# Kernel tuning notes

Measured on AMD Instinct MI355X. Metric: run time of the kernel, lower is better.

The kernel has to match this reference:

```python
import jax, jax.numpy as jnp
import numpy as np

NUM_HEADS = 8
EPS = 1e-5


def setup_inputs() -> dict:
    key = jax.random.key(0)
    k1, k2, k3 = jax.random.split(key, 3)
    C = 512
    x = jax.random.normal(k1, (16, C, 32, 32), dtype=jnp.float32)
    # 1x1 conv1d weights stored as [out, in] (kernel size 1 squeezed)
    w_qkv = jax.random.normal(k2, (3 * C, C), dtype=jnp.float32) * (1.0 / np.sqrt(C))
    b_qkv = jnp.zeros((3 * C,), dtype=jnp.float32)
    w_proj = jax.random.normal(k3, (C, C), dtype=jnp.float32) * (1.0 / np.sqrt(C))
    b_proj = jnp.zeros((C,), dtype=jnp.float32)
    return {"x": x, "w_qkv": w_qkv, "b_qkv": b_qkv, "w_proj": w_proj, "b_proj": b_proj}


def reference(x, w_qkv, b_qkv, w_proj, b_proj):
    b, c, H, W = x.shape
    T = H * W
    xf = x.reshape(b, c, T)
    # z_normalize over spatial dim (dim 2..) per (batch, channel), biased var
    mean = jnp.mean(xf, axis=2, keepdims=True)
    var = jnp.var(xf, axis=2, keepdims=True)
    xn = (xf - mean) / jnp.sqrt(var + EPS)
    # 1x1 conv: qkv projection -> [b, 3c, T]
    qkv = jnp.einsum('oc,bct->bot', w_qkv, xn) + b_qkv[None, :, None]
    ch = c // NUM_HEADS
    # legacy layout: [b, H*3*C, T] -> [b*H, 3*ch, T] -> split
    qkv = qkv.reshape(b * NUM_HEADS, 3 * ch, T)
    q, k, v = qkv[:, :ch], qkv[:, ch:2 * ch], qkv[:, 2 * ch:]
    scale = 1.0 / np.sqrt(np.sqrt(ch)).astype(np.float32)
    weight = jnp.einsum('bct,bcs->bts', q * scale, k * scale)  # [b*H, T, T]
    weight = jax.nn.softmax(weight.astype(jnp.float32), axis=-1).astype(q.dtype)
    a = jnp.einsum('bts,bcs->bct', weight, v).reshape(b, c, T)
    h = jnp.einsum('oc,bct->bot', w_proj, a) + b_proj[None, :, None]
    return (xn + h).reshape(b, c, H, W)
```

## Files before the change

kernel.cpp:

```cpp
#include <hip/hip_runtime.h>
#include <hip/hip_bf16.h>

using bf16x8s = __attribute__((ext_vector_type(8))) short;
using f32x4   = __attribute__((ext_vector_type(4))) float;
using f32x16  = __attribute__((ext_vector_type(16))) float;
using u32x4   = __attribute__((ext_vector_type(4))) unsigned int;

#define DEVI __device__ __forceinline__

static constexpr int BB  = 16;
static constexpr int CC  = 512;
static constexpr int TT  = 1024;
static constexpr int OQ  = 1536;
static constexpr int NH  = 8;
static constexpr int CHD = 64;

DEVI void load_lds16(const void* g, void* l) {
  __builtin_amdgcn_global_load_lds((const __attribute__((address_space(1))) void*)g,
                                   (__attribute__((address_space(3))) void*)l,
                                   16, 0, 0);
}

DEVI unsigned int cvtpk_bf16(float lo, float hi) {
  unsigned int r;
  asm("v_cvt_pk_bf16_f32 %0, %1, %2" : "=v"(r) : "v"(lo), "v"(hi));
  return r;
}

DEVI void plswap(unsigned int a, unsigned int b, unsigned int& x, unsigned int& y) {
#if __has_builtin(__builtin_amdgcn_permlane32_swap)
  auto r = __builtin_amdgcn_permlane32_swap((int)a, (int)b, false, false);
  x = (unsigned int)r[0];
  y = (unsigned int)r[1];
#else
  unsigned int pa = (unsigned int)__shfl_xor((int)a, 32);
  unsigned int pb = (unsigned int)__shfl_xor((int)b, 32);
  const bool hi = (threadIdx.x & 32) != 0;
  x = hi ? pb : a;
  y = hi ? b : pa;
#endif
}

__global__ __launch_bounds__(256) void k_convert_w(const float* __restrict__ wq,
                                                   const float* __restrict__ wp,
                                                   __hip_bfloat16* __restrict__ wqb,
                                                   __hip_bfloat16* __restrict__ wpb) {
  int i = blockIdx.x * 256 + threadIdx.x;
  const int NQ = OQ * CC;
  if (i < NQ) wqb[i] = __float2bfloat16(wq[i]);
  else        wpb[i - NQ] = __float2bfloat16(wp[i - NQ]);
}

__global__ __launch_bounds__(256) void k_ln_stats(const float* __restrict__ x,
                                                  float* __restrict__ mean,
                                                  float* __restrict__ rstd) {
  const int row = blockIdx.x;
  const float4* xv = (const float4*)(x + (size_t)row * TT);
  float4 v = xv[threadIdx.x];
  float s = v.x + v.y + v.z + v.w;
  float q = v.x * v.x + v.y * v.y + v.z * v.z + v.w * v.w;
  #pragma unroll
  for (int off = 1; off < 64; off <<= 1) {
    s += __shfl_xor(s, off);
    q += __shfl_xor(q, off);
  }
  __shared__ float ss[4], sq[4];
  const int wave = threadIdx.x >> 6;
  if ((threadIdx.x & 63) == 0) { ss[wave] = s; sq[wave] = q; }
  __syncthreads();
  if (threadIdx.x == 0) {
    float S = ss[0] + ss[1] + ss[2] + ss[3];
    float Q = sq[0] + sq[1] + sq[2] + sq[3];
    float m = S * (1.0f / TT);
    float var = Q * (1.0f / TT) - m * m;
    mean[row] = m;
    rstd[row] = 1.0f / sqrtf(var + 1e-5f);
  }
}

__global__ __launch_bounds__(256) void k_normT(const float* __restrict__ x,
                                               const float* __restrict__ mean,
                                               const float* __restrict__ rstd,
                                               __hip_bfloat16* __restrict__ xnT) {
  const int t0 = blockIdx.x * 64;
  const int c0 = blockIdx.y * 64;
  const int b  = blockIdx.z;
  __shared__ __hip_bfloat16 tile[64][66];
  const int tl = threadIdx.x & 63;
  const int cb = (threadIdx.x >> 6) * 16;
  #pragma unroll
  for (int i = 0; i < 16; ++i) {
    const int cl = cb + i;
    const int gc = b * CC + c0 + cl;
    float v = x[(size_t)gc * TT + t0 + tl];
    float xn = (v - mean[gc]) * rstd[gc];
    tile[tl][cl] = __float2bfloat16(xn);
  }
  __syncthreads();
  #pragma unroll
  for (int i = 0; i < 16; ++i) {
    const int tl2 = cb + i;
    const int cl2 = tl;
    xnT[((size_t)(b * TT + t0 + tl2)) * CC + c0 + cl2] = tile[tl2][cl2];
  }
}

__global__ __launch_bounds__(256) void k_qkv_gemm(const __hip_bfloat16* __restrict__ Wq,
                                                  const __hip_bfloat16* __restrict__ Xt,
                                                  const float* __restrict__ bias,
                                                  __hip_bfloat16* __restrict__ Qb,
                                                  __hip_bfloat16* __restrict__ Kb,
                                                  __hip_bfloat16* __restrict__ Vb) {
  __shared__ __hip_bfloat16 As[128 * 64];
  __shared__ __hip_bfloat16 Bs[128 * 64];
  const int tid  = threadIdx.x;
  const int lane = tid & 63;
  const int wave = tid >> 6;
  const int wr = wave >> 1, wc = wave & 1;
  const int tn0 = blockIdx.x * 128;
  const int om0 = blockIdx.y * 128;
  const int b   = blockIdx.z;

  const __hip_bfloat16* Ab  = Wq + (size_t)om0 * CC;
  const __hip_bfloat16* Bbp = Xt + ((size_t)b * TT + tn0) * CC;

  f32x4 acc[4][4] = {};
  const int l15  = lane & 15;
  const int kgrp = (lane >> 4) << 3;

  for (int k0 = 0; k0 < CC; k0 += 64) {
    #pragma unroll
    for (int r = 0; r < 4; ++r) {
      int idx = r * 256 + tid;
      int row = idx >> 3, ch = (idx & 7) << 3;
      load_lds16(Ab + (size_t)row * CC + k0 + ch, &As[(r * 256 + wave * 64) * 8]);
    }
    #pragma unroll
    for (int r = 0; r < 4; ++r) {
      int idx = r * 256 + tid;
      int row = idx >> 3, ch = (idx & 7) << 3;
      load_lds16(Bbp + (size_t)row * CC + k0 + ch, &Bs[(r * 256 + wave * 64) * 8]);
    }
    __syncthreads();
    #pragma unroll
    for (int kk = 0; kk < 2; ++kk) {
      const int klo = kk * 32 + kgrp;
      bf16x8s af[4], bfr[4];
      #pragma unroll
      for (int mf = 0; mf < 4; ++mf)
        af[mf] = *(const bf16x8s*)&As[(wr * 64 + mf * 16 + l15) * 64 + klo];
      #pragma unroll
      for (int nf = 0; nf < 4; ++nf)
        bfr[nf] = *(const bf16x8s*)&Bs[(wc * 64 + nf * 16 + l15) * 64 + klo];
      #pragma unroll
      for (int mf = 0; mf < 4; ++mf)
        #pragma unroll
        for (int nf = 0; nf < 4; ++nf)
          acc[mf][nf] = __builtin_amdgcn_mfma_f32_16x16x32_bf16(af[mf], bfr[nf], acc[mf][nf], 0, 0, 0);
    }
    __syncthreads();
  }

  const int rg = (lane >> 4) << 2;
  #pragma unroll
  for (int mf = 0; mf < 4; ++mf) {
    #pragma unroll
    for (int j = 0; j < 4; ++j) {
      const int o  = om0 + wr * 64 + mf * 16 + rg + j;
      const int h  = o / 192;
      const int r  = o % 192;
      const int bh = b * NH + h;
      const float bv = bias[o];
      #pragma unroll
      for (int nf = 0; nf < 4; ++nf) {
        const int t = tn0 + wc * 64 + nf * 16 + l15;
        float val = acc[mf][nf][j] + bv;
        if (r < 64)       Qb[((size_t)bh * TT + t) * CHD + r]        = __float2bfloat16(val * 0.125f);
        else if (r < 128) Kb[((size_t)bh * TT + t) * CHD + (r - 64)] = __float2bfloat16(val);
        else              Vb[((size_t)bh * CHD + (r - 128)) * TT + t] = __float2bfloat16(val);
      }
    }
  }
}

__global__ __launch_bounds__(256) void k_attn(const __hip_bfloat16* __restrict__ Qb,
                                              const __hip_bfloat16* __restrict__ Kb,
                                              const __hip_bfloat16* __restrict__ Vb,
                                              __hip_bfloat16* __restrict__ aT) {
  const int lane = threadIdx.x & 63;
  const int wave = threadIdx.x >> 6;
  const int bh   = blockIdx.y;
  const int q0   = blockIdx.x * 128 + wave * 32;
  const int l31  = lane & 31;
  const int hi8  = (lane >> 5) << 3;

  __shared__ char lds[2][16384];

  const __hip_bfloat16* Qh = Qb + (size_t)bh * TT * CHD;
  const __hip_bfloat16* Kh = Kb + (size_t)bh * TT * CHD;
  const __hip_bfloat16* Vh = Vb + (size_t)bh * CHD * TT;

  auto stage = [&](int buf, int kv0) {
    const char* kg = (const char*)(Kh + (size_t)kv0 * CHD);
    const char* vg = (const char*)Vh + (size_t)kv0 * 2;
    #pragma unroll
    for (int i = 0; i < 2; ++i) {
      const int slot = wave * 128 + i * 64 + lane;
      const int o = slot * 16;
      const int r = o >> 7;
      const int cs = o & 127;
      const int swc = cs ^ ((r & 7) << 4);
      load_lds16(kg + (o & ~127) + swc, &lds[buf][(wave * 128 + i * 64) * 16]);
      load_lds16(vg + r * 2048 + swc,   &lds[buf][8192 + (wave * 128 + i * 64) * 16]);
    }
  };

  bf16x8s aq[4];
  #pragma unroll
  for (int d = 0; d < 4; ++d)
    aq[d] = *(const bf16x8s*)&Qh[(size_t)(q0 + l31) * CHD + d * 16 + hi8];

  f32x16 oacc0 = {}, oacc1 = {};
  float m_run = -1e30f, l_run = 0.f;

  const int sw = (l31 & 7) << 4;
  const int cb = hi8 * 2;

  stage(0, 0);
  __syncthreads();

  for (int st = 0; st < 16; ++st) {
    const int buf = st & 1;
    if (st < 15) stage(buf ^ 1, (st + 1) * 64);

    const char* kb = lds[buf];
    const char* vb = lds[buf] + 8192;

    bf16x8s kf0[4], kf1[4];
    #pragma unroll
    for (int d = 0; d < 4; ++d) {
      const int col = d * 32 + cb;
      kf0[d] = *(const bf16x8s*)(kb + l31 * 128        + (col ^ sw));
      kf1[d] = *(const bf16x8s*)(kb + (32 + l31) * 128 + (col ^ sw));
    }

    f32x16 s0 = {}, s1 = {};
    __builtin_amdgcn_s_setprio(1);
    #pragma unroll
    for (int d = 0; d < 4; ++d) {
      s0 = __builtin_amdgcn_mfma_f32_32x32x16_bf16(kf0[d], aq[d], s0, 0, 0, 0);
      s1 = __builtin_amdgcn_mfma_f32_32x32x16_bf16(kf1[d], aq[d], s1, 0, 0, 0);
    }
    __builtin_amdgcn_s_setprio(0);

    bf16x8s vf0[4], vf1[4];
    #pragma unroll
    for (int ks = 0; ks < 4; ++ks) {
      const int col = ks * 32 + cb;
      vf0[ks] = *(const bf16x8s*)(vb + l31 * 128        + (col ^ sw));
      vf1[ks] = *(const bf16x8s*)(vb + (32 + l31) * 128 + (col ^ sw));
    }

    float t16[16];
    #pragma unroll
    for (int i = 0; i < 16; ++i) t16[i] = fmaxf(s0[i], s1[i]);
    float t8[8];
    #pragma unroll
    for (int i = 0; i < 8; ++i) t8[i] = fmaxf(t16[i], t16[i + 8]);
    float t4[4];
    #pragma unroll
    for (int i = 0; i < 4; ++i) t4[i] = fmaxf(t8[i], t8[i + 4]);
    float lmax = fmaxf(fmaxf(t4[0], t4[1]), fmaxf(t4[2], t4[3]));
    float pmax = fmaxf(lmax, __shfl_xor(lmax, 32));

    if (!__all(pmax <= m_run + 8.0f)) {
      const float mnew  = fmaxf(m_run, pmax);
      const float alpha = __expf(m_run - mnew);
      m_run = mnew;
      l_run *= alpha;
      #pragma unroll
      for (int i = 0; i < 16; ++i) { oacc0[i] *= alpha; oacc1[i] *= alpha; }
    }

    #pragma unroll
    for (int i = 0; i < 16; ++i) s0[i] = __expf(s0[i] - m_run);
    #pragma unroll
    for (int i = 0; i < 16; ++i) s1[i] = __expf(s1[i] - m_run);
    float a8[8];
    #pragma unroll
    for (int i = 0; i < 8; ++i) a8[i] = (s0[i] + s0[i + 8]) + (s1[i] + s1[i + 8]);
    float a4[4];
    #pragma unroll
    for (int i = 0; i < 4; ++i) a4[i] = a8[i] + a8[i + 4];
    float lsum = (a4[0] + a4[1]) + (a4[2] + a4[3]);
    lsum += __shfl_xor(lsum, 32);
    l_run += lsum;

    unsigned int wa[8], wb[8];
    #pragma unroll
    for (int g = 0; g < 4; ++g) {
      wa[g]     = cvtpk_bf16(s0[4 * g + 0], s0[4 * g + 1]);
      wb[g]     = cvtpk_bf16(s0[4 * g + 2], s0[4 * g + 3]);
      wa[g + 4] = cvtpk_bf16(s1[4 * g + 0], s1[4 * g + 1]);
      wb[g + 4] = cvtpk_bf16(s1[4 * g + 2], s1[4 * g + 3]);
    }

    __builtin_amdgcn_s_setprio(1);
    #pragma unroll
    for (int ks = 0; ks < 4; ++ks) {
      unsigned int x0, y0, x1, y1;
      plswap(wa[2 * ks], wa[2 * ks + 1], x0, y0);
      plswap(wb[2 * ks], wb[2 * ks + 1], x1, y1);
      bf16x8s pf = __builtin_bit_cast(bf16x8s, (u32x4){x0, x1, y0, y1});
      oacc0 = __builtin_amdgcn_mfma_f32_32x32x16_bf16(vf0[ks], pf, oacc0, 0, 0, 0);
      oacc1 = __builtin_amdgcn_mfma_f32_32x32x16_bf16(vf1[ks], pf, oacc1, 0, 0, 0);
    }
    __builtin_amdgcn_s_setprio(0);

    __syncthreads();
  }

  const int b = bh >> 3, h = bh & 7;
  const float rl = 1.0f / l_run;
  const int t = q0 + l31;
  __hip_bfloat16* arow = aT + ((size_t)(b * TT + t)) * CC + h * CHD;
  const int hi4 = hi8 >> 1;
  #pragma unroll
  for (int rr = 0; rr < 4; ++rr) {
    {
      const int c0 = rr * 8 + hi4;
      unsigned int lo = cvtpk_bf16(oacc0[4 * rr + 0] * rl, oacc0[4 * rr + 1] * rl);
      unsigned int hw = cvtpk_bf16(oacc0[4 * rr + 2] * rl, oacc0[4 * rr + 3] * rl);
      *(uint2*)&arow[c0] = make_uint2(lo, hw);
    }
    {
      const int c0 = 32 + rr * 8 + hi4;
      unsigned int lo = cvtpk_bf16(oacc1[4 * rr + 0] * rl, oacc1[4 * rr + 1] * rl);
      unsigned int hw = cvtpk_bf16(oacc1[4 * rr + 2] * rl, oacc1[4 * rr + 3] * rl);
      *(uint2*)&arow[c0] = make_uint2(lo, hw);
    }
  }
}

__global__ __launch_bounds__(256) void k_proj_gemm(const __hip_bfloat16* __restrict__ Wp,
                                                   const __hip_bfloat16* __restrict__ At,
                                                   const float* __restrict__ bias,
                                                   const float* __restrict__ x,
                                                   const float* __restrict__ mean,
                                                   const float* __restrict__ rstd,
                                                   float* __restrict__ out) {
  __shared__ __hip_bfloat16 As[128 * 64];
  __shared__ __hip_bfloat16 Bs[128 * 64];
  const int tid  = threadIdx.x;
  const int lane = tid & 63;
  const int wave = tid >> 6;
  const int wr = wave >> 1, wc = wave & 1;
  const int tn0 = blockIdx.x * 128;
  const int om0 = blockIdx.y * 128;
  const int b   = blockIdx.z;

  const __hip_bfloat16* Ab  = Wp + (size_t)om0 * CC;
  const __hip_bfloat16* Bbp = At + ((size_t)b * TT + tn0) * CC;

  f32x4 acc[4][4] = {};
  const int l15  = lane & 15;
  const int kgrp = (lane >> 4) << 3;

  for (int k0 = 0; k0 < CC; k0 += 64) {
    #pragma unroll
    for (int r = 0; r < 4; ++r) {
      int idx = r * 256 + tid;
      int row = idx >> 3, ch = (idx & 7) << 3;
      load_lds16(Ab + (size_t)row * CC + k0 + ch, &As[(r * 256 + wave * 64) * 8]);
    }
    #pragma unroll
    for (int r = 0; r < 4; ++r) {
      int idx = r * 256 + tid;
      int row = idx >> 3, ch = (idx & 7) << 3;
      load_lds16(Bbp + (size_t)row * CC + k0 + ch, &Bs[(r * 256 + wave * 64) * 8]);
    }
    __syncthreads();
    #pragma unroll
    for (int kk = 0; kk < 2; ++kk) {
      const int klo = kk * 32 + kgrp;
      bf16x8s af[4], bfr[4];
      #pragma unroll
      for (int mf = 0; mf < 4; ++mf)
        af[mf] = *(const bf16x8s*)&As[(wr * 64 + mf * 16 + l15) * 64 + klo];
      #pragma unroll
      for (int nf = 0; nf < 4; ++nf)
        bfr[nf] = *(const bf16x8s*)&Bs[(wc * 64 + nf * 16 + l15) * 64 + klo];
      #pragma unroll
      for (int mf = 0; mf < 4; ++mf)
        #pragma unroll
        for (int nf = 0; nf < 4; ++nf)
          acc[mf][nf] = __builtin_amdgcn_mfma_f32_16x16x32_bf16(af[mf], bfr[nf], acc[mf][nf], 0, 0, 0);
    }
    __syncthreads();
  }

  const int rg = (lane >> 4) << 2;
  #pragma unroll
  for (int mf = 0; mf < 4; ++mf) {
    #pragma unroll
    for (int j = 0; j < 4; ++j) {
      const int o = om0 + wr * 64 + mf * 16 + rg + j;
      const int gco = b * CC + o;
      const float bv = bias[o];
      const float mu = mean[gco], rs = rstd[gco];
      #pragma unroll
      for (int nf = 0; nf < 4; ++nf) {
        const int t = tn0 + wc * 64 + nf * 16 + l15;
        const size_t xi = (size_t)gco * TT + t;
        float xn = (x[xi] - mu) * rs;
        out[xi] = xn + acc[mf][nf][j] + bv;
      }
    }
  }
}

extern "C" void kernel_launch(void* const* d_in, const int* in_sizes, int n_in,
                              void* d_out, int out_size, void* d_ws, size_t ws_size,
                              hipStream_t stream) {
  const float* x  = (const float*)d_in[0];
  const float* wq = (const float*)d_in[1];
  const float* bq = (const float*)d_in[2];
  const float* wp = (const float*)d_in[3];
  const float* bp = (const float*)d_in[4];
  float* out = (float*)d_out;

  char* ws = (char*)d_ws;
  __hip_bfloat16* wqb = (__hip_bfloat16*)(ws);
  __hip_bfloat16* wpb = (__hip_bfloat16*)(ws + 1572864);
  float*          mean = (float*)(ws + 2097152);
  float*          rstd = (float*)(ws + 2129920);
  __hip_bfloat16* xnT = (__hip_bfloat16*)(ws + 2162688);
  __hip_bfloat16* Qb  = (__hip_bfloat16*)(ws + 18939904);
  __hip_bfloat16* Kb  = (__hip_bfloat16*)(ws + 35717120);
  __hip_bfloat16* Vb  = (__hip_bfloat16*)(ws + 52494336);
  __hip_bfloat16* aT  = xnT;

  k_convert_w<<<4096, 256, 0, stream>>>(wq, wp, wqb, wpb);
  k_ln_stats<<<BB * CC, 256, 0, stream>>>(x, mean, rstd);
  k_normT<<<dim3(TT / 64, CC / 64, BB), 256, 0, stream>>>(x, mean, rstd, xnT);
  k_qkv_gemm<<<dim3(TT / 128, OQ / 128, BB), 256, 0, stream>>>(wqb, xnT, bq, Qb, Kb, Vb);
  k_attn<<<dim3(TT / 128, BB * NH), 256, 0, stream>>>(Qb, Kb, Vb, aT);
  k_proj_gemm<<<dim3(TT / 128, CC / 128, BB), 256, 0, stream>>>(wpb, aT, bp, x, mean, rstd, out);
}
```

Baseline: 250.1 us.

## Double-buffer LDS with XOR swizzle in QKV and projection GEMMs

Both 1x1-conv GEMM kernels now use two LDS buffers of K=32 tiles, so the global-to-LDS loads for the next tile are issued before the MFMAs on the current one, instead of load-sync-compute with K=64. LDS columns are XOR-swizzled by row to reduce bank conflicts on the fragment reads. The change halves the K step per barrier and doubles the iteration count, which adds sync overhead. There is also one barrier per iteration, so correctness depends on that barrier covering the buffer reuse.

```diff
diff --git a/kernel.cpp b/kernel.cpp
--- a/kernel.cpp
+++ b/kernel.cpp
@@ -105,14 +105,15 @@
   }
 }
 
+
 __global__ __launch_bounds__(256) void k_qkv_gemm(const __hip_bfloat16* __restrict__ Wq,
                                                   const __hip_bfloat16* __restrict__ Xt,
                                                   const float* __restrict__ bias,
                                                   __hip_bfloat16* __restrict__ Qb,
                                                   __hip_bfloat16* __restrict__ Kb,
                                                   __hip_bfloat16* __restrict__ Vb) {
-  __shared__ __hip_bfloat16 As[128 * 64];
-  __shared__ __hip_bfloat16 Bs[128 * 64];
+  __shared__ __hip_bfloat16 As2[2][128 * 32];
+  __shared__ __hip_bfloat16 Bs2[2][128 * 32];
   const int tid  = threadIdx.x;
   const int lane = tid & 63;
   const int wave = tid >> 6;
@@ -121,43 +122,55 @@
   const int om0 = blockIdx.y * 128;
   const int b   = blockIdx.z;
 
-  const __hip_bfloat16* Ab  = Wq + (size_t)om0 * CC;
-  const __hip_bfloat16* Bbp = Xt + ((size_t)b * TT + tn0) * CC;
+  const char* Ab  = (const char*)(Wq + (size_t)om0 * CC);
+  const char* Bbp = (const char*)(Xt + ((size_t)b * TT + tn0) * CC);
 
   f32x4 acc[4][4] = {};
   const int l15  = lane & 15;
-  const int kgrp = (lane >> 4) << 3;
-
-  for (int k0 = 0; k0 < CC; k0 += 64) {
-    #pragma unroll
-    for (int r = 0; r < 4; ++r) {
-      int idx = r * 256 + tid;
-      int row = idx >> 3, ch = (idx & 7) << 3;
-      load_lds16(Ab + (size_t)row * CC + k0 + ch, &As[(r * 256 + wave * 64) * 8]);
-    }
-    #pragma unroll
-    for (int r = 0; r < 4; ++r) {
-      int idx = r * 256 + tid;
-      int row = idx >> 3, ch = (idx & 7) << 3;
-      load_lds16(Bbp + (size_t)row * CC + k0 + ch, &Bs[(r * 256 + wave * 64) * 8]);
-    }
-    __syncthreads();
-    #pragma unroll
-    for (int kk = 0; kk < 2; ++kk) {
-      const int klo = kk * 32 + kgrp;
-      bf16x8s af[4], bfr[4];
-      #pragma unroll
-      for (int mf = 0; mf < 4; ++mf)
-        af[mf] = *(const bf16x8s*)&As[(wr * 64 + mf * 16 + l15) * 64 + klo];
+  const int frc  = ((lane >> 4) << 3) * 2;
+  const int rsw  = ((l15 >> 1) & 3) << 4;
+
+  int srow[2], scsw[2], sdst[2];
+  #pragma unroll
+  for (int i = 0; i < 2; ++i) {
+    const int o = (i * 256 + tid) * 16;
+    const int r = o >> 6, c = o & 63;
+    srow[i] = r;
+    scsw[i] = c ^ (((r >> 1) & 3) << 4);
+    sdst[i] = (i * 256 + wave * 64) * 16;
+  }
+
+  auto stage = [&](int buf, int k0) {
+    const int kb = k0 * 2;
+    #pragma unroll
+    for (int i = 0; i < 2; ++i) {
+      load_lds16(Ab  + (size_t)srow[i] * 1024 + kb + scsw[i], (char*)As2[buf] + sdst[i]);
+      load_lds16(Bbp + (size_t)srow[i] * 1024 + kb + scsw[i], (char*)Bs2[buf] + sdst[i]);
+    }
+  };
+
+  stage(0, 0);
+  __syncthreads();
+
+  for (int kt = 0; kt < 16; ++kt) {
+    const int buf = kt & 1;
+    if (kt < 15) stage(buf ^ 1, (kt + 1) * 32);
+
+    const char* Asb = (const char*)As2[buf];
+    const char* Bsb = (const char*)Bs2[buf];
+    bf16x8s af[4], bfr[4];
+    #pragma unroll
+    for (int mf = 0; mf < 4; ++mf)
+      af[mf] = *(const bf16x8s*)(Asb + (wr * 64 + mf * 16 + l15) * 64 + (frc ^ rsw));
+    #pragma unroll
+    for (int nf = 0; nf < 4; ++nf)
+      bfr[nf] = *(const bf16x8s*)(Bsb + (wc * 64 + nf * 16 + l15) * 64 + (frc ^ rsw));
+    #pragma unroll
+    for (int mf = 0; mf < 4; ++mf)
       #pragma unroll
       for (int nf = 0; nf < 4; ++nf)
-        bfr[nf] = *(const bf16x8s*)&Bs[(wc * 64 + nf * 16 + l15) * 64 + klo];
-      #pragma unroll
-      for (int mf = 0; mf < 4; ++mf)
-        #pragma unroll
-        for (int nf = 0; nf < 4; ++nf)
-          acc[mf][nf] = __builtin_amdgcn_mfma_f32_16x16x32_bf16(af[mf], bfr[nf], acc[mf][nf], 0, 0, 0);
-    }
+        acc[mf][nf] = __builtin_amdgcn_mfma_f32_16x16x32_bf16(af[mf], bfr[nf], acc[mf][nf], 0, 0, 0);
+
     __syncthreads();
   }
 
@@ -349,8 +362,8 @@
                                                    const float* __restrict__ mean,
                                                    const float* __restrict__ rstd,
                                                    float* __restrict__ out) {
-  __shared__ __hip_bfloat16 As[128 * 64];
-  __shared__ __hip_bfloat16 Bs[128 * 64];
+  __shared__ __hip_bfloat16 As2[2][128 * 32];
+  __shared__ __hip_bfloat16 Bs2[2][128 * 32];
   const int tid  = threadIdx.x;
   const int lane = tid & 63;
   const int wave = tid >> 6;
@@ -359,43 +372,55 @@
   const int om0 = blockIdx.y * 128;
   const int b   = blockIdx.z;
 
-  const __hip_bfloat16* Ab  = Wp + (size_t)om0 * CC;
-  const __hip_bfloat16* Bbp = At + ((size_t)b * TT + tn0) * CC;
+  const char* Ab  = (const char*)(Wp + (size_t)om0 * CC);
+  const char* Bbp = (const char*)(At + ((size_t)b * TT + tn0) * CC);
 
   f32x4 acc[4][4] = {};
   const int l15  = lane & 15;
-  const int kgrp = (lane >> 4) << 3;
-
-  for (int k0 = 0; k0 < CC; k0 += 64) {
-    #pragma unroll
-    for (int r = 0; r < 4; ++r) {
-      int idx = r * 256 + tid;
-      int row = idx >> 3, ch = (idx & 7) << 3;
-      load_lds16(Ab + (size_t)row * CC + k0 + ch, &As[(r * 256 + wave * 64) * 8]);
-    }
-    #pragma unroll
-    for (int r = 0; r < 4; ++r) {
-      int idx = r * 256 + tid;
-      int row = idx >> 3, ch = (idx & 7) << 3;
-      load_lds16(Bbp + (size_t)row * CC + k0 + ch, &Bs[(r * 256 + wave * 64) * 8]);
-    }
-    __syncthreads();
-    #pragma unroll
-    for (int kk = 0; kk < 2; ++kk) {
-      const int klo = kk * 32 + kgrp;
-      bf16x8s af[4], bfr[4];
-      #pragma unroll
-      for (int mf = 0; mf < 4; ++mf)
-        af[mf] = *(const bf16x8s*)&As[(wr * 64 + mf * 16 + l15) * 64 + klo];
+  const int frc  = ((lane >> 4) << 3) * 2;
+  const int rsw  = ((l15 >> 1) & 3) << 4;
+
+  int srow[2], scsw[2], sdst[2];
+  #pragma unroll
+  for (int i = 0; i < 2; ++i) {
+    const int o = (i * 256 + tid) * 16;
+    const int r = o >> 6, c = o & 63;
+    srow[i] = r;
+    scsw[i] = c ^ (((r >> 1) & 3) << 4);
+    sdst[i] = (i * 256 + wave * 64) * 16;
+  }
+
+  auto stage = [&](int buf, int k0) {
+    const int kb = k0 * 2;
+    #pragma unroll
+    for (int i = 0; i < 2; ++i) {
+      load_lds16(Ab  + (size_t)srow[i] * 1024 + kb + scsw[i], (char*)As2[buf] + sdst[i]);
+      load_lds16(Bbp + (size_t)srow[i] * 1024 + kb + scsw[i], (char*)Bs2[buf] + sdst[i]);
+    }
+  };
+
+  stage(0, 0);
+  __syncthreads();
+
+  for (int kt = 0; kt < 16; ++kt) {
+    const int buf = kt & 1;
+    if (kt < 15) stage(buf ^ 1, (kt + 1) * 32);
+
+    const char* Asb = (const char*)As2[buf];
+    const char* Bsb = (const char*)Bs2[buf];
+    bf16x8s af[4], bfr[4];
+    #pragma unroll
+    for (int mf = 0; mf < 4; ++mf)
+      af[mf] = *(const bf16x8s*)(Asb + (wr * 64 + mf * 16 + l15) * 64 + (frc ^ rsw));
+    #pragma unroll
+    for (int nf = 0; nf < 4; ++nf)
+      bfr[nf] = *(const bf16x8s*)(Bsb + (wc * 64 + nf * 16 + l15) * 64 + (frc ^ rsw));
+    #pragma unroll
+    for (int mf = 0; mf < 4; ++mf)
       #pragma unroll
       for (int nf = 0; nf < 4; ++nf)
-        bfr[nf] = *(const bf16x8s*)&Bs[(wc * 64 + nf * 16 + l15) * 64 + klo];
-      #pragma unroll
-      for (int mf = 0; mf < 4; ++mf)
-        #pragma unroll
-        for (int nf = 0; nf < 4; ++nf)
-          acc[mf][nf] = __builtin_amdgcn_mfma_f32_16x16x32_bf16(af[mf], bfr[nf], acc[mf][nf], 0, 0, 0);
-    }
+        acc[mf][nf] = __builtin_amdgcn_mfma_f32_16x16x32_bf16(af[mf], bfr[nf], acc[mf][nf], 0, 0, 0);
+
     __syncthreads();
   }
 
```

Measured after the change: 248.9 us. No clear change (-0.5%).
